# Kernel optimization log

Hardware: AMD Instinct MI355X
Metric: run time of the kernel (lower is better)

The kernel has to match this reference:

```python
import jax, jax.numpy as jnp
from jax import lax
import numpy as np

N_TOOLS = 50
DIM = 512
N_TOKENS = 8192
PARAM_DIM = 256


def setup_inputs() -> dict:
    key = jax.random.key(0)
    ks = jax.random.split(key, 8)
    s = 1.0 / np.sqrt(DIM)
    x = jax.random.normal(ks[0], (N_TOKENS, DIM), dtype=jnp.float32)
    router_w = jax.random.uniform(ks[1], (N_TOOLS, DIM), jnp.float32, -s, s)
    router_b = jax.random.uniform(ks[2], (N_TOOLS,), jnp.float32, -s, s)
    expert_w = jax.random.uniform(ks[3], (N_TOOLS, DIM, DIM), jnp.float32, -s, s)
    expert_b = jax.random.uniform(ks[4], (N_TOOLS, DIM), jnp.float32, -s, s)
    param_w = jax.random.uniform(ks[5], (PARAM_DIM, DIM), jnp.float32, -s, s)
    param_b = jax.random.uniform(ks[6], (PARAM_DIM,), jnp.float32, -s, s)
    return {"x": x, "router_w": router_w, "router_b": router_b,
            "expert_w": expert_w, "expert_b": expert_b,
            "param_w": param_w, "param_b": param_b}


def _moe_adapt(x, tool_idx, expert_w, expert_b):
    # Top-1 dispatch: for each expert i, y_i = x @ W_i.T + b_i, written only
    # where tool_idx == i. Scan over the fixed 50 experts (mirrors the torch
    # masked per-expert Linear loop) with masked select instead of scatter.
    def step(acc, wb):
        i, W, b = wb
        y = x @ W.T + b  # [N, dim]
        mask = (tool_idx == i)[:, None]
        return jnp.where(mask, y, acc), None

    init = jnp.zeros_like(x)
    acc, _ = lax.scan(step, init, (jnp.arange(N_TOOLS), expert_w, expert_b))
    return acc


def reference(x, router_w, router_b, expert_w, expert_b, param_w, param_b):
    tool_logits = x @ router_w.T + router_b            # [N, 50]
    tool_probs = jax.nn.softmax(tool_logits, axis=-1)   # [N, 50]
    tool_idx = jnp.argmax(tool_probs, axis=-1)          # [N] int
    adapted = _moe_adapt(x, tool_idx, expert_w, expert_b)  # [N, dim]
    params = x @ param_w.T + param_b                    # [N, 256]
    return (tool_idx, tool_probs, adapted, params)
```

## Files before the change

kernel.cpp:

```cpp
#include <hip/hip_runtime.h>
#include <hip/hip_bf16.h>
#include <math.h>

#define N_TOKENS 8192
#define DIM      512
#define N_TOOLS  50
#define PARAM_DIM 256
#define N_ROWBLK (N_TOKENS / 64)
#define MAX_BATCHES 192
#define LDSS 72

typedef float  f32x4 __attribute__((ext_vector_type(4)));
typedef short  s16x8 __attribute__((ext_vector_type(8)));
typedef short  s16x4 __attribute__((ext_vector_type(4)));

#define WS_IDX     0
#define WS_HIST    8192
#define WS_PHIST   14592
#define WS_OFFSETS 20992
#define WS_COUNTS  21056
#define WS_ORDER   21120
#define WS_BE      29312
#define WS_BM0     29504
#define WS_NB      29696
#define WS_XH      32768
#define WS_XL      2130944

__device__ inline float bf2f(short s) {
    return __uint_as_float(((unsigned)(unsigned short)s) << 16);
}

__device__ inline s16x4 pk4(float a, float b, float c, float d) {
    __hip_bfloat162 p0 = __float22bfloat162_rn(make_float2(a, b));
    __hip_bfloat162 p1 = __float22bfloat162_rn(make_float2(c, d));
    union { __hip_bfloat162 h; short2 s; } u0, u1;
    u0.h = p0; u1.h = p1;
    s16x4 r; r[0] = u0.s.x; r[1] = u0.s.y; r[2] = u1.s.x; r[3] = u1.s.y;
    return r;
}

__global__ __launch_bounds__(256) void cvt_x_kernel(const float* __restrict__ x,
                                                    short* __restrict__ xh,
                                                    short* __restrict__ xl) {
    size_t i = (size_t)(blockIdx.x * 256 + threadIdx.x) * 4;
    float4 v = *(const float4*)&x[i];
    s16x4 h = pk4(v.x, v.y, v.z, v.w);
    s16x4 l = pk4(v.x - bf2f(h[0]), v.y - bf2f(h[1]),
                  v.z - bf2f(h[2]), v.w - bf2f(h[3]));
    *(s16x4*)&xh[i] = h;
    *(s16x4*)&xl[i] = l;
}

__global__ __launch_bounds__(256) void head_mfma(const short* __restrict__ xh,
                                                 const short* __restrict__ xl,
                                                 const float* __restrict__ pw,
                                                 const float* __restrict__ pb,
                                                 const float* __restrict__ rw,
                                                 const float* __restrict__ rb,
                                                 float* __restrict__ out_params,
                                                 float* __restrict__ probs,
                                                 float* __restrict__ out_idx,
                                                 int* __restrict__ idx_i,
                                                 int* __restrict__ hist) {
    int r0 = blockIdx.y * 64;
    bool isl = (blockIdx.x == 4);
    int c0 = isl ? 0 : blockIdx.x * 64;

    __shared__ short As[64 * LDSS];
    __shared__ short Bs[64 * LDSS];
    __shared__ short Al[64 * LDSS];
    __shared__ short Bl[64 * LDSS];
    __shared__ int rowcol[64];

    int tid = threadIdx.x;
    int wv = tid >> 6;
    int lane = tid & 63;
    int fm = lane & 15;
    int q = lane >> 4;

    const float* Bsrc = isl ? rw : pw;

    int ar0 = tid >> 3, ag = tid & 7;
    int ar1 = ar0 + 32;
    const short* aptr0 = xh + (size_t)(r0 + ar0) * DIM + ag * 8;
    const short* aptr1 = xh + (size_t)(r0 + ar1) * DIM + ag * 8;
    const short* alptr0 = xl + (size_t)(r0 + ar0) * DIM + ag * 8;
    const short* alptr1 = xl + (size_t)(r0 + ar1) * DIM + ag * 8;
    int bc[4], bg[4];
    const float* bptr[4];
#pragma unroll
    for (int i = 0; i < 4; ++i) {
        int u = i * 256 + tid;
        bc[i] = u >> 4; bg[i] = u & 15;
        bptr[i] = Bsrc + (size_t)(c0 + bc[i]) * DIM + bg[i] * 4;
    }

    f32x4 acc[4] = {{0.f, 0.f, 0.f, 0.f}, {0.f, 0.f, 0.f, 0.f},
                    {0.f, 0.f, 0.f, 0.f}, {0.f, 0.f, 0.f, 0.f}};

    s16x8 apre0, apre1, alpre0, alpre1;
    float4 bpre[4];
    apre0 = *(const s16x8*)aptr0;
    apre1 = *(const s16x8*)aptr1;
    if (isl) { alpre0 = *(const s16x8*)alptr0; alpre1 = *(const s16x8*)alptr1; }
#pragma unroll
    for (int i = 0; i < 4; ++i) {
        float4 v = {0.f, 0.f, 0.f, 0.f};
        if (!isl || bc[i] < N_TOOLS) v = *(const float4*)bptr[i];
        bpre[i] = v;
    }

    for (int k0 = 0; k0 < DIM; k0 += 64) {
        *(s16x8*)&As[ar0 * LDSS + ag * 8] = apre0;
        *(s16x8*)&As[ar1 * LDSS + ag * 8] = apre1;
        if (isl) {
            *(s16x8*)&Al[ar0 * LDSS + ag * 8] = alpre0;
            *(s16x8*)&Al[ar1 * LDSS + ag * 8] = alpre1;
        }
#pragma unroll
        for (int i = 0; i < 4; ++i) {
            float4 v = bpre[i];
            s16x4 h = pk4(v.x, v.y, v.z, v.w);
            *(s16x4*)&Bs[bc[i] * LDSS + bg[i] * 4] = h;
            if (isl) {
                s16x4 l = pk4(v.x - bf2f(h[0]), v.y - bf2f(h[1]),
                              v.z - bf2f(h[2]), v.w - bf2f(h[3]));
                *(s16x4*)&Bl[bc[i] * LDSS + bg[i] * 4] = l;
            }
        }
        __syncthreads();

        int kn = k0 + 64;
        if (kn < DIM) {
            apre0 = *(const s16x8*)(aptr0 + kn);
            apre1 = *(const s16x8*)(aptr1 + kn);
            if (isl) {
                alpre0 = *(const s16x8*)(alptr0 + kn);
                alpre1 = *(const s16x8*)(alptr1 + kn);
            }
#pragma unroll
            for (int i = 0; i < 4; ++i) {
                float4 v = {0.f, 0.f, 0.f, 0.f};
                if (!isl || bc[i] < N_TOOLS) v = *(const float4*)(bptr[i] + kn);
                bpre[i] = v;
            }
        }

#pragma unroll
        for (int kk = 0; kk < 64; kk += 32) {
            int ao = (wv * 16 + fm) * LDSS + kk + q * 8;
            s16x8 a = *(const s16x8*)&As[ao];
            if (!isl) {
#pragma unroll
                for (int n = 0; n < 4; ++n) {
                    s16x8 b = *(const s16x8*)&Bs[(n * 16 + fm) * LDSS + kk + q * 8];
                    acc[n] = __builtin_amdgcn_mfma_f32_16x16x32_bf16(a, b, acc[n], 0, 0, 0);
                }
            } else {
                s16x8 al = *(const s16x8*)&Al[ao];
#pragma unroll
                for (int n = 0; n < 4; ++n) {
                    int bo = (n * 16 + fm) * LDSS + kk + q * 8;
                    s16x8 b  = *(const s16x8*)&Bs[bo];
                    s16x8 bl = *(const s16x8*)&Bl[bo];
                    acc[n] = __builtin_amdgcn_mfma_f32_16x16x32_bf16(a,  b,  acc[n], 0, 0, 0);
                    acc[n] = __builtin_amdgcn_mfma_f32_16x16x32_bf16(a,  bl, acc[n], 0, 0, 0);
                    acc[n] = __builtin_amdgcn_mfma_f32_16x16x32_bf16(al, b,  acc[n], 0, 0, 0);
                }
            }
        }
        __syncthreads();
    }

    if (!isl) {
        float bias[4];
#pragma unroll
        for (int n = 0; n < 4; ++n) bias[n] = pb[c0 + n * 16 + fm];
#pragma unroll
        for (int r = 0; r < 4; ++r) {
            int row = r0 + wv * 16 + q * 4 + r;
            float* op = out_params + (size_t)row * PARAM_DIM + c0;
#pragma unroll
            for (int n = 0; n < 4; ++n) op[n * 16 + fm] = acc[n][r] + bias[n];
        }
    } else {
        float rbv[4];
#pragma unroll
        for (int n = 0; n < 4; ++n) {
            int c = n * 16 + fm;
            rbv[n] = (c < N_TOOLS) ? rb[c] : 0.f;
        }
#pragma unroll
        for (int rr = 0; rr < 4; ++rr) {
            int row_l = wv * 16 + q * 4 + rr;
            int row = r0 + row_l;
            float v[4];
            float vmax = -INFINITY; int vcol = N_TOOLS;
#pragma unroll
            for (int n = 0; n < 4; ++n) {
                int c = n * 16 + fm;
                v[n] = acc[n][rr] + rbv[n];
                if (c < N_TOOLS && v[n] > vmax) { vmax = v[n]; vcol = c; }
            }
#pragma unroll
            for (int s = 1; s < 16; s <<= 1) {
                float om = __shfl_xor(vmax, s, 64);
                int   oc = __shfl_xor(vcol, s, 64);
                if (om > vmax || (om == vmax && oc < vcol)) { vmax = om; vcol = oc; }
            }
            float e[4]; float esum = 0.f;
#pragma unroll
            for (int n = 0; n < 4; ++n) {
                int c = n * 16 + fm;
                e[n] = (c < N_TOOLS) ? expf(v[n] - vmax) : 0.f;
                esum += e[n];
            }
#pragma unroll
            for (int s = 1; s < 16; s <<= 1) esum += __shfl_xor(esum, s, 64);
            float inv = 1.f / esum;
#pragma unroll
            for (int n = 0; n < 4; ++n) {
                int c = n * 16 + fm;
                if (c < N_TOOLS) probs[(size_t)row * N_TOOLS + c] = e[n] * inv;
            }
            if (fm == 0) {
                out_idx[row] = (float)vcol;
                idx_i[row] = vcol;
                rowcol[row_l] = vcol;
            }
        }
        __syncthreads();
        if (wv == 0) {
            int myc = rowcol[lane];
            int cnt = 0;
            for (int e2 = 0; e2 < N_TOOLS; ++e2) {
                unsigned long long m = __ballot(myc == e2);
                if (lane == e2) cnt = __popcll(m);
            }
            if (lane < N_TOOLS) hist[blockIdx.y * N_TOOLS + lane] = cnt;
        }
    }
}

__global__ void scan1_kernel(const int* __restrict__ hist,
                             int* __restrict__ phist,
                             int* __restrict__ counts) {
    int e = blockIdx.x;
    int l = threadIdx.x;
    int v0 = hist[l * N_TOOLS + e];
    int v1 = hist[(64 + l) * N_TOOLS + e];
    int s0 = v0;
#pragma unroll
    for (int s = 1; s < 64; s <<= 1) {
        int t = __shfl_up(s0, s, 64);
        if (l >= s) s0 += t;
    }
    int tot0 = __shfl(s0, 63, 64);
    int s1 = v1;
#pragma unroll
    for (int s = 1; s < 64; s <<= 1) {
        int t = __shfl_up(s1, s, 64);
        if (l >= s) s1 += t;
    }
    s1 += tot0;
    phist[l * N_TOOLS + e] = s0 - v0;
    phist[(64 + l) * N_TOOLS + e] = s1 - v1;
    if (l == 63) counts[e] = s1;
}

__global__ void scan2_kernel(const int* __restrict__ counts,
                             int* __restrict__ offsets,
                             int* __restrict__ batch_e,
                             int* __restrict__ batch_m0,
                             int* __restrict__ nb_out) {
    int lane = threadIdx.x;
    int c = (lane < N_TOOLS) ? counts[lane] : 0;
    int pre = c;
#pragma unroll
    for (int s = 1; s < 64; s <<= 1) {
        int v = __shfl_up(pre, s, 64);
        if (lane >= s) pre += v;
    }
    if (lane < N_TOOLS) offsets[lane] = pre - c;

    int nb_i = (lane < N_TOOLS) ? (c + 63) >> 6 : 0;
    int pre2 = nb_i;
#pragma unroll
    for (int s = 1; s < 64; s <<= 1) {
        int v = __shfl_up(pre2, s, 64);
        if (lane >= s) pre2 += v;
    }
    int bstart = pre2 - nb_i;
    for (int b = 0; b < nb_i; ++b) {
        batch_e[bstart + b] = lane;
        batch_m0[bstart + b] = b * 64;
    }
    if (lane == 63) nb_out[0] = pre2;
}

__global__ void reorder_kernel(const int* __restrict__ idx_i,
                               const int* __restrict__ offsets,
                               const int* __restrict__ phist,
                               int* __restrict__ order) {
    int b = blockIdx.x;
    int lane = threadIdx.x;
    int t = b * 64 + lane;
    int e = idx_i[t];
    unsigned long long lt = (1ull << lane) - 1ull;
    int rank = 0;
    for (int ex = 0; ex < N_TOOLS; ++ex) {
        unsigned long long m = __ballot(e == ex);
        if (e == ex) rank = __popcll(m & lt);
    }
    order[offsets[e] + phist[b * N_TOOLS + e] + rank] = t;
}

__global__ __launch_bounds__(256) void adapted_mfma(const short* __restrict__ xh,
                                                    const float* __restrict__ ew,
                                                    const float* __restrict__ eb,
                                                    const int* __restrict__ order,
                                                    const int* __restrict__ batch_e,
                                                    const int* __restrict__ batch_m0,
                                                    const int* __restrict__ nb_ptr,
                                                    const int* __restrict__ offsets,
                                                    const int* __restrict__ counts,
                                                    float* __restrict__ out) {
    int b = blockIdx.y;
    if (b >= nb_ptr[0]) return;
    int e = batch_e[b];
    int m0 = batch_m0[b];
    int c0 = blockIdx.x * 64;
    int start = offsets[e] + m0;
    int len = counts[e] - m0;
    if (len > 64) len = 64;

    __shared__ short As[64 * LDSS];
    __shared__ short Bs[64 * LDSS];
    __shared__ int toks[64];

    int tid = threadIdx.x;
    if (tid < 64) toks[tid] = (tid < len) ? order[start + tid] : -1;
    __syncthreads();

    int wv = tid >> 6;
    int lane = tid & 63;
    int fm = lane & 15;
    int q = lane >> 4;

    const float* We = ew + (size_t)e * DIM * DIM;

    int ar0 = tid >> 3, ag = tid & 7;
    int ar1 = ar0 + 32;
    int tok0 = toks[ar0], tok1 = toks[ar1];
    const short* aptr0 = (tok0 >= 0) ? xh + (size_t)tok0 * DIM + ag * 8 : nullptr;
    const short* aptr1 = (tok1 >= 0) ? xh + (size_t)tok1 * DIM + ag * 8 : nullptr;
    int bc[4], bg[4];
    const float* bptr[4];
#pragma unroll
    for (int i = 0; i < 4; ++i) {
        int u = i * 256 + tid;
        bc[i] = u >> 4; bg[i] = u & 15;
        bptr[i] = We + (size_t)(c0 + bc[i]) * DIM + bg[i] * 4;
    }

    f32x4 acc[4] = {{0.f, 0.f, 0.f, 0.f}, {0.f, 0.f, 0.f, 0.f},
                    {0.f, 0.f, 0.f, 0.f}, {0.f, 0.f, 0.f, 0.f}};

    const s16x8 z8 = {0, 0, 0, 0, 0, 0, 0, 0};
    s16x8 apre0 = aptr0 ? *(const s16x8*)aptr0 : z8;
    s16x8 apre1 = aptr1 ? *(const s16x8*)aptr1 : z8;
    float4 bpre[4];
#pragma unroll
    for (int i = 0; i < 4; ++i) bpre[i] = *(const float4*)bptr[i];

    for (int k0 = 0; k0 < DIM; k0 += 64) {
        *(s16x8*)&As[ar0 * LDSS + ag * 8] = apre0;
        *(s16x8*)&As[ar1 * LDSS + ag * 8] = apre1;
#pragma unroll
        for (int i = 0; i < 4; ++i) {
            float4 v = bpre[i];
            *(s16x4*)&Bs[bc[i] * LDSS + bg[i] * 4] = pk4(v.x, v.y, v.z, v.w);
        }
        __syncthreads();

        int kn = k0 + 64;
        if (kn < DIM) {
            apre0 = aptr0 ? *(const s16x8*)(aptr0 + kn) : z8;
            apre1 = aptr1 ? *(const s16x8*)(aptr1 + kn) : z8;
#pragma unroll
            for (int i = 0; i < 4; ++i) bpre[i] = *(const float4*)(bptr[i] + kn);
        }

#pragma unroll
        for (int kk = 0; kk < 64; kk += 32) {
            s16x8 a = *(const s16x8*)&As[(wv * 16 + fm) * LDSS + kk + q * 8];
#pragma unroll
            for (int n = 0; n < 4; ++n) {
                s16x8 bf = *(const s16x8*)&Bs[(n * 16 + fm) * LDSS + kk + q * 8];
                acc[n] = __builtin_amdgcn_mfma_f32_16x16x32_bf16(a, bf, acc[n], 0, 0, 0);
            }
        }
        __syncthreads();
    }

    float bias[4];
#pragma unroll
    for (int n = 0; n < 4; ++n) bias[n] = eb[(size_t)e * DIM + c0 + n * 16 + fm];

#pragma unroll
    for (int r = 0; r < 4; ++r) {
        int row = wv * 16 + q * 4 + r;
        int tok = toks[row];
        if (tok < 0) continue;
        float* op = out + (size_t)tok * DIM + c0;
#pragma unroll
        for (int n = 0; n < 4; ++n) op[n * 16 + fm] = acc[n][r] + bias[n];
    }
}

extern "C" void kernel_launch(void* const* d_in, const int* in_sizes, int n_in,
                              void* d_out, int out_size, void* d_ws, size_t ws_size,
                              hipStream_t stream) {
    const float* x        = (const float*)d_in[0];
    const float* router_w = (const float*)d_in[1];
    const float* router_b = (const float*)d_in[2];
    const float* expert_w = (const float*)d_in[3];
    const float* expert_b = (const float*)d_in[4];
    const float* param_w  = (const float*)d_in[5];
    const float* param_b  = (const float*)d_in[6];

    float* out = (float*)d_out;
    float* out_idx     = out;
    float* out_probs   = out + N_TOKENS;
    float* out_adapted = out + N_TOKENS + N_TOKENS * N_TOOLS;
    float* out_params  = out_adapted + (size_t)N_TOKENS * DIM;

    int* ws = (int*)d_ws;
    int* ws_idx     = ws + WS_IDX;
    int* ws_hist    = ws + WS_HIST;
    int* ws_phist   = ws + WS_PHIST;
    int* ws_offsets = ws + WS_OFFSETS;
    int* ws_counts  = ws + WS_COUNTS;
    int* ws_order   = ws + WS_ORDER;
    int* ws_be      = ws + WS_BE;
    int* ws_bm0     = ws + WS_BM0;
    int* ws_nb      = ws + WS_NB;
    short* ws_xh    = (short*)(ws + WS_XH);
    short* ws_xl    = (short*)(ws + WS_XL);

    cvt_x_kernel<<<N_TOKENS * DIM / 4 / 256, 256, 0, stream>>>(x, ws_xh, ws_xl);

    head_mfma<<<dim3(5, N_ROWBLK), 256, 0, stream>>>(ws_xh, ws_xl, param_w, param_b,
                                                     router_w, router_b,
                                                     out_params, out_probs,
                                                     out_idx, ws_idx, ws_hist);

    scan1_kernel<<<N_TOOLS, 64, 0, stream>>>(ws_hist, ws_phist, ws_counts);

    scan2_kernel<<<1, 64, 0, stream>>>(ws_counts, ws_offsets, ws_be, ws_bm0, ws_nb);

    reorder_kernel<<<N_ROWBLK, 64, 0, stream>>>(ws_idx, ws_offsets, ws_phist, ws_order);

    adapted_mfma<<<dim3(8, MAX_BATCHES), 256, 0, stream>>>(ws_xh, expert_w, expert_b,
                                                           ws_order, ws_be, ws_bm0, ws_nb,
                                                           ws_offsets, ws_counts, out_adapted);
}
```

Before: 154.6 us.

## Pre-convert head weights, atomic expert histogram, and 128-row expert tiles

Converts param and router weights to bf16 (hi/lo split for router) once in a merged conversion kernel, so head_mfma no longer converts fp32 weights in every block. The per-block histogram and two scan kernels are replaced by global atomic counts, a single prefix kernel, and an atomic-cursor reorder using LDS atomics. The expert GEMM tile grows from 64 to 128 tokens, with each wave doing two M subtiles, so each converted expert weight tile is reused across more tokens and fewer batches launch. Token order within each expert now depends on atomic ordering, and the larger tile costs more registers and LDS and wastes more rows on partially filled batches.

```diff
diff --git a/kernel.cpp b/kernel.cpp
--- a/kernel.cpp
+++ b/kernel.cpp
@@ -7,7 +7,8 @@
 #define N_TOOLS  50
 #define PARAM_DIM 256
 #define N_ROWBLK (N_TOKENS / 64)
-#define MAX_BATCHES 192
+#define MAX_BATCHES 128
+#define TM 128
 #define LDSS 72
 
 typedef float  f32x4 __attribute__((ext_vector_type(4)));
@@ -15,16 +16,18 @@
 typedef short  s16x4 __attribute__((ext_vector_type(4)));
 
 #define WS_IDX     0
-#define WS_HIST    8192
-#define WS_PHIST   14592
-#define WS_OFFSETS 20992
-#define WS_COUNTS  21056
-#define WS_ORDER   21120
-#define WS_BE      29312
-#define WS_BM0     29504
-#define WS_NB      29696
-#define WS_XH      32768
-#define WS_XL      2130944
+#define WS_COUNTS  8192
+#define WS_CURSOR  8256
+#define WS_OFFSETS 8320
+#define WS_BE      8384
+#define WS_BM0     8512
+#define WS_NB      8640
+#define WS_ORDER   8704
+#define WS_PWH     16896
+#define WS_RWH     82432
+#define WS_RWL     98816
+#define WS_XH      115200
+#define WS_XL      2212352
 
 __device__ inline float bf2f(short s) {
     return __uint_as_float(((unsigned)(unsigned short)s) << 16);
@@ -39,29 +42,60 @@
     return r;
 }
 
-__global__ __launch_bounds__(256) void cvt_x_kernel(const float* __restrict__ x,
-                                                    short* __restrict__ xh,
-                                                    short* __restrict__ xl) {
-    size_t i = (size_t)(blockIdx.x * 256 + threadIdx.x) * 4;
-    float4 v = *(const float4*)&x[i];
-    s16x4 h = pk4(v.x, v.y, v.z, v.w);
-    s16x4 l = pk4(v.x - bf2f(h[0]), v.y - bf2f(h[1]),
-                  v.z - bf2f(h[2]), v.w - bf2f(h[3]));
-    *(s16x4*)&xh[i] = h;
-    *(s16x4*)&xl[i] = l;
+#define CVT_XB  4096
+#define CVT_PWB 128
+#define CVT_RWB 32
+#define CVT_GRID (CVT_XB + CVT_PWB + CVT_RWB + 1)
+__global__ __launch_bounds__(256) void cvt_kernel(const float* __restrict__ x,
+                                                  const float* __restrict__ pw,
+                                                  const float* __restrict__ rw,
+                                                  short* __restrict__ xh,
+                                                  short* __restrict__ xl,
+                                                  short* __restrict__ pwh,
+                                                  short* __restrict__ rwh,
+                                                  short* __restrict__ rwl,
+                                                  int* __restrict__ counts) {
+    int bid = blockIdx.x;
+    int tid = threadIdx.x;
+    if (bid < CVT_XB) {
+        size_t i = ((size_t)bid * 256 + tid) * 4;
+        float4 v = *(const float4*)&x[i];
+        s16x4 h = pk4(v.x, v.y, v.z, v.w);
+        s16x4 l = pk4(v.x - bf2f(h[0]), v.y - bf2f(h[1]),
+                      v.z - bf2f(h[2]), v.w - bf2f(h[3]));
+        *(s16x4*)&xh[i] = h;
+        *(s16x4*)&xl[i] = l;
+    } else if (bid < CVT_XB + CVT_PWB) {
+        size_t i = ((size_t)(bid - CVT_XB) * 256 + tid) * 4;
+        float4 v = *(const float4*)&pw[i];
+        *(s16x4*)&pwh[i] = pk4(v.x, v.y, v.z, v.w);
+    } else if (bid < CVT_XB + CVT_PWB + CVT_RWB) {
+        int i = ((bid - CVT_XB - CVT_PWB) * 256 + tid) * 4;
+        int row = i >> 9;
+        float4 v = {0.f, 0.f, 0.f, 0.f};
+        if (row < N_TOOLS) v = *(const float4*)&rw[i];
+        s16x4 h = pk4(v.x, v.y, v.z, v.w);
+        s16x4 l = pk4(v.x - bf2f(h[0]), v.y - bf2f(h[1]),
+                      v.z - bf2f(h[2]), v.w - bf2f(h[3]));
+        *(s16x4*)&rwh[i] = h;
+        *(s16x4*)&rwl[i] = l;
+    } else {
+        if (tid < 64) counts[tid] = 0;
+    }
 }
 
 __global__ __launch_bounds__(256) void head_mfma(const short* __restrict__ xh,
                                                  const short* __restrict__ xl,
-                                                 const float* __restrict__ pw,
+                                                 const short* __restrict__ pwh,
                                                  const float* __restrict__ pb,
-                                                 const float* __restrict__ rw,
+                                                 const short* __restrict__ rwh,
+                                                 const short* __restrict__ rwl,
                                                  const float* __restrict__ rb,
                                                  float* __restrict__ out_params,
                                                  float* __restrict__ probs,
                                                  float* __restrict__ out_idx,
                                                  int* __restrict__ idx_i,
-                                                 int* __restrict__ hist) {
+                                                 int* __restrict__ counts) {
     int r0 = blockIdx.y * 64;
     bool isl = (blockIdx.x == 4);
     int c0 = isl ? 0 : blockIdx.x * 64;
@@ -77,8 +111,6 @@
     int lane = tid & 63;
     int fm = lane & 15;
     int q = lane >> 4;
-
-    const float* Bsrc = isl ? rw : pw;
 
     int ar0 = tid >> 3, ag = tid & 7;
     int ar1 = ar0 + 32;
@@ -86,47 +118,45 @@
     const short* aptr1 = xh + (size_t)(r0 + ar1) * DIM + ag * 8;
     const short* alptr0 = xl + (size_t)(r0 + ar0) * DIM + ag * 8;
     const short* alptr1 = xl + (size_t)(r0 + ar1) * DIM + ag * 8;
-    int bc[4], bg[4];
-    const float* bptr[4];
-#pragma unroll
-    for (int i = 0; i < 4; ++i) {
+
+    const short* bsrc = isl ? rwh : (pwh + (size_t)c0 * DIM);
+    int bc[2], bg[2];
+    const short* bph[2];
+    const short* bpl[2];
+#pragma unroll
+    for (int i = 0; i < 2; ++i) {
         int u = i * 256 + tid;
-        bc[i] = u >> 4; bg[i] = u & 15;
-        bptr[i] = Bsrc + (size_t)(c0 + bc[i]) * DIM + bg[i] * 4;
+        bc[i] = u >> 3; bg[i] = u & 7;
+        bph[i] = bsrc + (size_t)bc[i] * DIM + bg[i] * 8;
+        bpl[i] = rwl + (size_t)bc[i] * DIM + bg[i] * 8;
     }
 
     f32x4 acc[4] = {{0.f, 0.f, 0.f, 0.f}, {0.f, 0.f, 0.f, 0.f},
                     {0.f, 0.f, 0.f, 0.f}, {0.f, 0.f, 0.f, 0.f}};
 
     s16x8 apre0, apre1, alpre0, alpre1;
-    float4 bpre[4];
+    s16x8 bpre[2], blpre[2];
     apre0 = *(const s16x8*)aptr0;
     apre1 = *(const s16x8*)aptr1;
     if (isl) { alpre0 = *(const s16x8*)alptr0; alpre1 = *(const s16x8*)alptr1; }
 #pragma unroll
-    for (int i = 0; i < 4; ++i) {
-        float4 v = {0.f, 0.f, 0.f, 0.f};
-        if (!isl || bc[i] < N_TOOLS) v = *(const float4*)bptr[i];
-        bpre[i] = v;
+    for (int i = 0; i < 2; ++i) {
+        bpre[i] = *(const s16x8*)bph[i];
+        if (isl) blpre[i] = *(const s16x8*)bpl[i];
     }
 
     for (int k0 = 0; k0 < DIM; k0 += 64) {
         *(s16x8*)&As[ar0 * LDSS + ag * 8] = apre0;
         *(s16x8*)&As[ar1 * LDSS + ag * 8] = apre1;
+#pragma unroll
+        for (int i = 0; i < 2; ++i)
+            *(s16x8*)&Bs[bc[i] * LDSS + bg[i] * 8] = bpre[i];
         if (isl) {
             *(s16x8*)&Al[ar0 * LDSS + ag * 8] = alpre0;
             *(s16x8*)&Al[ar1 * LDSS + ag * 8] = alpre1;
-        }
-#pragma unroll
-        for (int i = 0; i < 4; ++i) {
-            float4 v = bpre[i];
-            s16x4 h = pk4(v.x, v.y, v.z, v.w);
-            *(s16x4*)&Bs[bc[i] * LDSS + bg[i] * 4] = h;
-            if (isl) {
-                s16x4 l = pk4(v.x - bf2f(h[0]), v.y - bf2f(h[1]),
-                              v.z - bf2f(h[2]), v.w - bf2f(h[3]));
-                *(s16x4*)&Bl[bc[i] * LDSS + bg[i] * 4] = l;
-            }
+#pragma unroll
+            for (int i = 0; i < 2; ++i)
+                *(s16x8*)&Bl[bc[i] * LDSS + bg[i] * 8] = blpre[i];
         }
         __syncthreads();
 
@@ -139,10 +169,9 @@
                 alpre1 = *(const s16x8*)(alptr1 + kn);
             }
 #pragma unroll
-            for (int i = 0; i < 4; ++i) {
-                float4 v = {0.f, 0.f, 0.f, 0.f};
-                if (!isl || bc[i] < N_TOOLS) v = *(const float4*)(bptr[i] + kn);
-                bpre[i] = v;
+            for (int i = 0; i < 2; ++i) {
+                bpre[i] = *(const s16x8*)(bph[i] + kn);
+                if (isl) blpre[i] = *(const s16x8*)(bpl[i] + kn);
             }
         }
 
@@ -237,39 +266,14 @@
                 unsigned long long m = __ballot(myc == e2);
                 if (lane == e2) cnt = __popcll(m);
             }
-            if (lane < N_TOOLS) hist[blockIdx.y * N_TOOLS + lane] = cnt;
-        }
-    }
-}
-
-__global__ void scan1_kernel(const int* __restrict__ hist,
-                             int* __restrict__ phist,
-                             int* __restrict__ counts) {
-    int e = blockIdx.x;
-    int l = threadIdx.x;
-    int v0 = hist[l * N_TOOLS + e];
-    int v1 = hist[(64 + l) * N_TOOLS + e];
-    int s0 = v0;
-#pragma unroll
-    for (int s = 1; s < 64; s <<= 1) {
-        int t = __shfl_up(s0, s, 64);
-        if (l >= s) s0 += t;
-    }
-    int tot0 = __shfl(s0, 63, 64);
-    int s1 = v1;
-#pragma unroll
-    for (int s = 1; s < 64; s <<= 1) {
-        int t = __shfl_up(s1, s, 64);
-        if (l >= s) s1 += t;
-    }
-    s1 += tot0;
-    phist[l * N_TOOLS + e] = s0 - v0;
-    phist[(64 + l) * N_TOOLS + e] = s1 - v1;
-    if (l == 63) counts[e] = s1;
-}
-
-__global__ void scan2_kernel(const int* __restrict__ counts,
+            if (lane < N_TOOLS && cnt > 0) atomicAdd(&counts[lane], cnt);
+        }
+    }
+}
+
+__global__ void plumb_kernel(const int* __restrict__ counts,
                              int* __restrict__ offsets,
+                             int* __restrict__ cursor,
                              int* __restrict__ batch_e,
                              int* __restrict__ batch_m0,
                              int* __restrict__ nb_out) {
@@ -281,9 +285,9 @@
         int v = __shfl_up(pre, s, 64);
         if (lane >= s) pre += v;
     }
-    if (lane < N_TOOLS) offsets[lane] = pre - c;
-
-    int nb_i = (lane < N_TOOLS) ? (c + 63) >> 6 : 0;
+    if (lane < N_TOOLS) { offsets[lane] = pre - c; cursor[lane] = pre - c; }
+
+    int nb_i = (lane < N_TOOLS) ? (c + TM - 1) / TM : 0;
     int pre2 = nb_i;
 #pragma unroll
     for (int s = 1; s < 64; s <<= 1) {
@@ -293,26 +297,26 @@
     int bstart = pre2 - nb_i;
     for (int b = 0; b < nb_i; ++b) {
         batch_e[bstart + b] = lane;
-        batch_m0[bstart + b] = b * 64;
+        batch_m0[bstart + b] = b * TM;
     }
     if (lane == 63) nb_out[0] = pre2;
 }
 
-__global__ void reorder_kernel(const int* __restrict__ idx_i,
-                               const int* __restrict__ offsets,
-                               const int* __restrict__ phist,
-                               int* __restrict__ order) {
-    int b = blockIdx.x;
-    int lane = threadIdx.x;
-    int t = b * 64 + lane;
+__global__ __launch_bounds__(256) void reorder_kernel(const int* __restrict__ idx_i,
+                                                      int* __restrict__ cursor,
+                                                      int* __restrict__ order) {
+    __shared__ int lcnt[N_TOOLS];
+    __shared__ int lbase[N_TOOLS];
+    int tid = threadIdx.x;
+    if (tid < N_TOOLS) lcnt[tid] = 0;
+    __syncthreads();
+    int t = blockIdx.x * 256 + tid;
     int e = idx_i[t];
-    unsigned long long lt = (1ull << lane) - 1ull;
-    int rank = 0;
-    for (int ex = 0; ex < N_TOOLS; ++ex) {
-        unsigned long long m = __ballot(e == ex);
-        if (e == ex) rank = __popcll(m & lt);
-    }
-    order[offsets[e] + phist[b * N_TOOLS + e] + rank] = t;
+    int r = atomicAdd(&lcnt[e], 1);
+    __syncthreads();
+    if (tid < N_TOOLS && lcnt[tid] > 0) lbase[tid] = atomicAdd(&cursor[tid], lcnt[tid]);
+    __syncthreads();
+    order[lbase[e] + r] = t;
 }
 
 __global__ __launch_bounds__(256) void adapted_mfma(const short* __restrict__ xh,
@@ -332,14 +336,14 @@
     int c0 = blockIdx.x * 64;
     int start = offsets[e] + m0;
     int len = counts[e] - m0;
-    if (len > 64) len = 64;
-
-    __shared__ short As[64 * LDSS];
+    if (len > TM) len = TM;
+
+    __shared__ short As[TM * LDSS];
     __shared__ short Bs[64 * LDSS];
-    __shared__ int toks[64];
+    __shared__ int toks[TM];
 
     int tid = threadIdx.x;
-    if (tid < 64) toks[tid] = (tid < len) ? order[start + tid] : -1;
+    if (tid < TM) toks[tid] = (tid < len) ? order[start + tid] : -1;
     __syncthreads();
 
     int wv = tid >> 6;
@@ -349,11 +353,14 @@
 
     const float* We = ew + (size_t)e * DIM * DIM;
 
-    int ar0 = tid >> 3, ag = tid & 7;
-    int ar1 = ar0 + 32;
-    int tok0 = toks[ar0], tok1 = toks[ar1];
-    const short* aptr0 = (tok0 >= 0) ? xh + (size_t)tok0 * DIM + ag * 8 : nullptr;
-    const short* aptr1 = (tok1 >= 0) ? xh + (size_t)tok1 * DIM + ag * 8 : nullptr;
+    int ag = tid & 7;
+    int ar[4]; const short* aptr[4];
+#pragma unroll
+    for (int i = 0; i < 4; ++i) {
+        ar[i] = i * 32 + (tid >> 3);
+        int tk = toks[ar[i]];
+        aptr[i] = (tk >= 0) ? xh + (size_t)tk * DIM + ag * 8 : nullptr;
+    }
     int bc[4], bg[4];
     const float* bptr[4];
 #pragma unroll
@@ -363,19 +370,21 @@
         bptr[i] = We + (size_t)(c0 + bc[i]) * DIM + bg[i] * 4;
     }
 
-    f32x4 acc[4] = {{0.f, 0.f, 0.f, 0.f}, {0.f, 0.f, 0.f, 0.f},
-                    {0.f, 0.f, 0.f, 0.f}, {0.f, 0.f, 0.f, 0.f}};
+    f32x4 acc[8] = {{0.f,0.f,0.f,0.f},{0.f,0.f,0.f,0.f},{0.f,0.f,0.f,0.f},{0.f,0.f,0.f,0.f},
+                    {0.f,0.f,0.f,0.f},{0.f,0.f,0.f,0.f},{0.f,0.f,0.f,0.f},{0.f,0.f,0.f,0.f}};
 
     const s16x8 z8 = {0, 0, 0, 0, 0, 0, 0, 0};
-    s16x8 apre0 = aptr0 ? *(const s16x8*)aptr0 : z8;
-    s16x8 apre1 = aptr1 ? *(const s16x8*)aptr1 : z8;
+    s16x8 apre[4];
     float4 bpre[4];
 #pragma unroll
+    for (int i = 0; i < 4; ++i) apre[i] = aptr[i] ? *(const s16x8*)aptr[i] : z8;
+#pragma unroll
     for (int i = 0; i < 4; ++i) bpre[i] = *(const float4*)bptr[i];
 
     for (int k0 = 0; k0 < DIM; k0 += 64) {
-        *(s16x8*)&As[ar0 * LDSS + ag * 8] = apre0;
-        *(s16x8*)&As[ar1 * LDSS + ag * 8] = apre1;
+#pragma unroll
+        for (int i = 0; i < 4; ++i)
+            *(s16x8*)&As[ar[i] * LDSS + ag * 8] = apre[i];
 #pragma unroll
         for (int i = 0; i < 4; ++i) {
             float4 v = bpre[i];
@@ -385,19 +394,21 @@
 
         int kn = k0 + 64;
         if (kn < DIM) {
-            apre0 = aptr0 ? *(const s16x8*)(aptr0 + kn) : z8;
-            apre1 = aptr1 ? *(const s16x8*)(aptr1 + kn) : z8;
+#pragma unroll
+            for (int i = 0; i < 4; ++i) apre[i] = aptr[i] ? *(const s16x8*)(aptr[i] + kn) : z8;
 #pragma unroll
             for (int i = 0; i < 4; ++i) bpre[i] = *(const float4*)(bptr[i] + kn);
         }
 
 #pragma unroll
         for (int kk = 0; kk < 64; kk += 32) {
-            s16x8 a = *(const s16x8*)&As[(wv * 16 + fm) * LDSS + kk + q * 8];
+            s16x8 a0 = *(const s16x8*)&As[(wv * 32 + fm) * LDSS + kk + q * 8];
+            s16x8 a1 = *(const s16x8*)&As[(wv * 32 + 16 + fm) * LDSS + kk + q * 8];
 #pragma unroll
             for (int n = 0; n < 4; ++n) {
                 s16x8 bf = *(const s16x8*)&Bs[(n * 16 + fm) * LDSS + kk + q * 8];
-                acc[n] = __builtin_amdgcn_mfma_f32_16x16x32_bf16(a, bf, acc[n], 0, 0, 0);
+                acc[n]     = __builtin_amdgcn_mfma_f32_16x16x32_bf16(a0, bf, acc[n],     0, 0, 0);
+                acc[4 + n] = __builtin_amdgcn_mfma_f32_16x16x32_bf16(a1, bf, acc[4 + n], 0, 0, 0);
             }
         }
         __syncthreads();
@@ -408,13 +419,16 @@
     for (int n = 0; n < 4; ++n) bias[n] = eb[(size_t)e * DIM + c0 + n * 16 + fm];
 
 #pragma unroll
-    for (int r = 0; r < 4; ++r) {
-        int row = wv * 16 + q * 4 + r;
-        int tok = toks[row];
-        if (tok < 0) continue;
-        float* op = out + (size_t)tok * DIM + c0;
-#pragma unroll
-        for (int n = 0; n < 4; ++n) op[n * 16 + fm] = acc[n][r] + bias[n];
+    for (int m = 0; m < 2; ++m) {
+#pragma unroll
+        for (int r = 0; r < 4; ++r) {
+            int row = wv * 32 + m * 16 + q * 4 + r;
+            int tok = toks[row];
+            if (tok < 0) continue;
+            float* op = out + (size_t)tok * DIM + c0;
+#pragma unroll
+            for (int n = 0; n < 4; ++n) op[n * 16 + fm] = acc[m * 4 + n][r] + bias[n];
+        }
     }
 }
 
@@ -437,29 +451,32 @@
 
     int* ws = (int*)d_ws;
     int* ws_idx     = ws + WS_IDX;
-    int* ws_hist    = ws + WS_HIST;
-    int* ws_phist   = ws + WS_PHIST;
+    int* ws_counts  = ws + WS_COUNTS;
+    int* ws_cursor  = ws + WS_CURSOR;
     int* ws_offsets = ws + WS_OFFSETS;
-    int* ws_counts  = ws + WS_COUNTS;
-    int* ws_order   = ws + WS_ORDER;
     int* ws_be      = ws + WS_BE;
     int* ws_bm0     = ws + WS_BM0;
     int* ws_nb      = ws + WS_NB;
+    int* ws_order   = ws + WS_ORDER;
+    short* ws_pwh   = (short*)(ws + WS_PWH);
+    short* ws_rwh   = (short*)(ws + WS_RWH);
+    short* ws_rwl   = (short*)(ws + WS_RWL);
     short* ws_xh    = (short*)(ws + WS_XH);
     short* ws_xl    = (short*)(ws + WS_XL);
 
-    cvt_x_kernel<<<N_TOKENS * DIM / 4 / 256, 256, 0, stream>>>(x, ws_xh, ws_xl);
-
-    head_mfma<<<dim3(5, N_ROWBLK), 256, 0, stream>>>(ws_xh, ws_xl, param_w, param_b,
-                                                     router_w, router_b,
+    cvt_kernel<<<CVT_GRID, 256, 0, stream>>>(x, param_w, router_w,
+                                             ws_xh, ws_xl, ws_pwh, ws_rwh, ws_rwl,
+                                             ws_counts);
+
+    head_mfma<<<dim3(5, N_ROWBLK), 256, 0, stream>>>(ws_xh, ws_xl, ws_pwh, param_b,
+                                                     ws_rwh, ws_rwl, router_b,
                                                      out_params, out_probs,
-                                                     out_idx, ws_idx, ws_hist);
-
-    scan1_kernel<<<N_TOOLS, 64, 0, stream>>>(ws_hist, ws_phist, ws_counts);
-
-    scan2_kernel<<<1, 64, 0, stream>>>(ws_counts, ws_offsets, ws_be, ws_bm0, ws_nb);
-
-    reorder_kernel<<<N_ROWBLK, 64, 0, stream>>>(ws_idx, ws_offsets, ws_phist, ws_order);
+                                                     out_idx, ws_idx, ws_counts);
+
+    plumb_kernel<<<1, 64, 0, stream>>>(ws_counts, ws_offsets, ws_cursor,
+                                       ws_be, ws_bm0, ws_nb);
+
+    reorder_kernel<<<N_TOKENS / 256, 256, 0, stream>>>(ws_idx, ws_cursor, ws_order);
 
     adapted_mfma<<<dim3(8, MAX_BATCHES), 256, 0, stream>>>(ws_xh, expert_w, expert_b,
                                                            ws_order, ws_be, ws_bm0, ws_nb,
```

Result: no change. 152.3 us (-1.4%).
